# Kernel optimization log

Measured on AMD Instinct MI355X. Metric: run time of the kernel, lower is better.

The kernel has to match this reference:

```python
import jax, jax.numpy as jnp
import numpy as np

K = 16          # max_points
S = 3           # num_scales
DM = 256        # d_model
KD = 16         # k_dim geometric projection
TAU = 1e-4
LN_EPS = 1e-5


def _boundaries():
    edges = [(i, j) for i in range(K) for j in range(i + 1, K)]
    tris = [(i, j, k) for i in range(K) for j in range(i + 1, K) for k in range(j + 1, K)]
    E, T = len(edges), len(tris)
    B1 = np.zeros((K, E), np.float32)
    for e, (i, j) in enumerate(edges):
        B1[i, e] = -1.0
        B1[j, e] = 1.0
    eidx = {e: n for n, e in enumerate(edges)}
    B2 = np.zeros((E, T), np.float32)
    for t, (i, j, k) in enumerate(tris):
        B2[eidx[(j, k)], t] = 1.0
        B2[eidx[(i, k)], t] = -1.0
        B2[eidx[(i, j)], t] = 1.0
    ei = np.array([e[0] for e in edges])
    ej = np.array([e[1] for e in edges])
    tij = np.array([eidx[(a, b)] for a, b, c in tris])
    tjk = np.array([eidx[(b, c)] for a, b, c in tris])
    tik = np.array([eidx[(a, c)] for a, b, c in tris])
    return (jnp.asarray(B1), jnp.asarray(B2), jnp.asarray(np.abs(B1)),
            jnp.asarray(ei), jnp.asarray(ej), jnp.asarray(tij), jnp.asarray(tjk), jnp.asarray(tik))

_B1, _B2, _ABS, _EI, _EJ, _TIJ, _TJK, _TIK = _boundaries()
E = _B1.shape[1]  # 120


def _ln(x, g, b):
    m = jnp.mean(x, -1, keepdims=True)
    v = jnp.mean((x - m) ** 2, -1, keepdims=True)
    return (x - m) * jax.lax.rsqrt(v + LN_EPS) * g + b


def setup_inputs() -> dict:
    key = jax.random.key(0)
    ks = jax.random.split(key, 12)
    B = 1024
    p = lambda k, *sh: 0.02 * jax.random.normal(k, sh, dtype=jnp.float32)
    return {
        'x': jax.random.normal(ks[0], (B, K, DM), dtype=jnp.float32),
        'mask': jnp.ones((B, K), dtype=jnp.float32),
        'Wg': p(ks[1], DM, KD), 'bg': jnp.zeros((KD,), jnp.float32),
        'log_scales': jnp.linspace(-1.5, 1.5, S, dtype=jnp.float32),
        'Wv': p(ks[2], DM, DM * S), 'bv': jnp.zeros((DM * S,), jnp.float32),
        'We': p(ks[3], DM, DM * S), 'be': jnp.zeros((DM * S,), jnp.float32),
        'Wo': p(ks[4], DM * S * 2, DM), 'bo': jnp.zeros((DM,), jnp.float32),
        'ln1_g': jnp.ones((DM,), jnp.float32), 'ln1_b': jnp.zeros((DM,), jnp.float32),
        'ln2_g': jnp.ones((DM,), jnp.float32), 'ln2_b': jnp.zeros((DM,), jnp.float32),
        'Wf1': p(ks[5], DM, DM * 4), 'bf1': jnp.zeros((DM * 4,), jnp.float32),
        'Wf2': p(ks[6], DM * 4, DM), 'bf2': jnp.zeros((DM,), jnp.float32),
    }


def reference(x, mask, Wg, bg, log_scales, Wv, bv, We, be, Wo, bo,
              ln1_g, ln1_b, ln2_g, ln2_b, Wf1, bf1, Wf2, bf2):
    B = x.shape[0]
    xn = _ln(x, ln1_g, ln1_b)
    P = xn @ Wg + bg                                   # [B,K,KD]
    m2 = mask[:, :, None] * mask[:, None, :]           # [B,K,K]
    p2 = jnp.sum(P * P, -1)
    Dsq = jnp.maximum(p2[:, :, None] + p2[:, None, :] - 2.0 * jnp.einsum('bkc,blc->bkl', P, P), 0.0) * m2
    sig2 = jnp.exp(log_scales) ** 2                    # [S]
    V0 = (xn @ Wv + bv).reshape(B, K, S, DM).transpose(0, 2, 1, 3)   # [B,S,K,D]
    Eraw = jnp.einsum('ke,bkd->bed', _ABS, xn)         # [B,E,D]
    Ein = (Eraw @ We + be).reshape(B, E, S, DM).transpose(0, 2, 1, 3)  # [B,S,E,D]
    aff = jnp.exp(-Dsq[:, None] / (2.0 * sig2[None, :, None, None] + 1e-8)) * m2[:, None]  # [B,S,K,K]
    W1 = aff[:, :, _EI, _EJ]                           # [B,S,E]
    W2 = W1[:, :, _TIJ] * W1[:, :, _TJK] * W1[:, :, _TIK]  # [B,S,T]
    L0 = jnp.einsum('ke,bse,le->bskl', _B1, W1, _B1) + TAU * jnp.eye(K, dtype=x.dtype)
    node_upd = jnp.einsum('bskl,bsld->bskd', L0, V0)
    term_down = jnp.einsum('ke,bk,kf->bef', _B1, mask, _B1)
    term_up = jnp.einsum('et,bst,ft->bsef', _B2, W2, _B2)
    L1 = term_down[:, None] + term_up + TAU * jnp.eye(E, dtype=x.dtype)
    edge_msg = jnp.einsum('bsef,bsfd->bsed', L1, Ein)
    edge_upd = jnp.einsum('ke,bsed->bskd', _ABS, edge_msg)
    nu = node_upd.transpose(0, 2, 1, 3).reshape(B, K, S * DM)
    eu = edge_upd.transpose(0, 2, 1, 3).reshape(B, K, S * DM)
    x = x + (jnp.concatenate([nu, eu], -1) @ Wo + bo)  # residual + attn_out (dropout=eval noop)
    h = _ln(x, ln2_g, ln2_b)
    return x + (jax.nn.gelu(h @ Wf1 + bf1, approximate=False) @ Wf2 + bf2)
```

## Files before the change

kernel.cpp:

```cpp
#include <hip/hip_runtime.h>
#include <hip/hip_bf16.h>
#include <cstdint>
#include <cstddef>

#define TAU 1e-4f
#define LN_EPS 1e-5f

typedef unsigned short ushort_t;
typedef unsigned int uint_t;
typedef __attribute__((ext_vector_type(8))) short short8;
typedef __attribute__((ext_vector_type(4))) float f32x4;

__device__ __forceinline__ ushort_t f2bf(float f) {
    union { float f; unsigned int u; } c; c.f = f;
    unsigned int r = (c.u + 0x7fffu + ((c.u >> 16) & 1u)) >> 16;
    return (ushort_t)r;
}
__device__ __forceinline__ float bf2f(ushort_t u) {
    union { unsigned int u; float f; } c; c.u = ((unsigned int)u) << 16;
    return c.f;
}
__device__ __forceinline__ void glds16(const void* g, void* l) {
    __builtin_amdgcn_global_load_lds((const __attribute__((address_space(1))) unsigned int*)g,
                                     (__attribute__((address_space(3))) unsigned int*)l,
                                     16, 0, 0);
}

__global__ __launch_bounds__(256) void kprep(
    const float* __restrict__ Wv, const float* __restrict__ We,
    const float* __restrict__ Wo, const float* __restrict__ bv,
    const float* __restrict__ be, const float* __restrict__ Wf1,
    const float* __restrict__ Wf2, ushort_t* __restrict__ WkT,
    ushort_t* __restrict__ Wf1T, ushort_t* __restrict__ Wf2T,
    float* __restrict__ cvpart, float* __restrict__ beWo) {
    __shared__ __align__(16) float S[64 * 65];
    const int tid = threadIdx.x;
    const int id = blockIdx.x;
    if (id < 384) {
        float (*rowS)[256] = (float(*)[256])S;
        const int q0 = (id & 63) * 4;
        const int w = id >> 6;
        const int half = w / 3, s = w - half * 3;
        const float* src = half ? We : Wv;
#pragma unroll
        for (int r = 0; r < 4; ++r)
            rowS[r][tid] = src[(size_t)(q0 + r) * 768 + s * 256 + tid];
        __syncthreads();
        const float* wo = Wo + (size_t)(half * 768 + s * 256) * 256 + tid;
        float a0 = 0.f, a1 = 0.f, a2 = 0.f, a3 = 0.f;
        for (int d = 0; d < 256; ++d) {
            float wv = wo[(size_t)d * 256];
            a0 += rowS[0][d] * wv; a1 += rowS[1][d] * wv;
            a2 += rowS[2][d] * wv; a3 += rowS[3][d] * wv;
        }
        const int rt = half * 3 + s;
        ushort4 pk;
        pk.x = f2bf(a0); pk.y = f2bf(a1); pk.z = f2bf(a2); pk.w = f2bf(a3);
        *(ushort4*)&WkT[(size_t)(rt * 256 + tid) * 256 + q0] = pk;
    } else if (id < 390) {
        const int w = id - 384;
        const int half = w / 3, s = w - half * 3;
        const float* vec = half ? be : bv;
        S[tid] = vec[s * 256 + tid];
        __syncthreads();
        const float* wo = Wo + (size_t)(half * 768 + s * 256) * 256 + tid;
        float acc = 0.f;
        for (int d = 0; d < 256; ++d) acc += S[d] * wo[(size_t)d * 256];
        if (half) beWo[s * 256 + tid] = acc;
        else cvpart[s * 256 + tid] = acc;
    } else {
        float (*tS)[65] = (float(*)[65])S;
        const float* src; ushort_t* dst;
        int sr0, sc0, ss, dr0, dc0, ds_;
        if (id < 454) {
            int t = id - 390; int ki = t & 3, ni = t >> 2;
            src = Wf1; ss = 1024; sr0 = ki * 64; sc0 = ni * 64;
            dst = Wf1T; ds_ = 256; dr0 = ni * 64; dc0 = ki * 64;
        } else {
            int t = id - 454; int ki = t >> 2, ni = t & 3;
            src = Wf2; ss = 256; sr0 = ki * 64; sc0 = ni * 64;
            dst = Wf2T; ds_ = 1024; dr0 = ni * 64; dc0 = ki * 64;
        }
        const int rl = tid >> 6, cl = tid & 63;
#pragma unroll
        for (int p = 0; p < 16; ++p) {
            int r = p * 4 + rl;
            tS[r][cl] = src[(size_t)(sr0 + r) * ss + sc0 + cl];
        }
        __syncthreads();
#pragma unroll
        for (int p = 0; p < 16; ++p) {
            int r = p * 4 + rl;
            dst[(size_t)(dr0 + r) * ds_ + dc0 + cl] = f2bf(tS[cl][r]);
        }
    }
}

__global__ __launch_bounds__(256) void kLN1G(
    const float* __restrict__ xg, const float* __restrict__ maskg,
    const float* __restrict__ Wg, const float* __restrict__ bg,
    const float* __restrict__ ls, const float* __restrict__ g1,
    const float* __restrict__ b1, ushort_t* __restrict__ xnbuf,
    float* __restrict__ Mbuf, float* __restrict__ gbuf) {
    __shared__ float XS[16][260];
    __shared__ __align__(16) float WB[16 * 260];
    __shared__ float Pl[16][17];
    __shared__ float dotm[16][17];
    __shared__ float mk[16];
    float (*WgT)[260] = (float(*)[260])WB;
    float (*DsqS)[17] = (float(*)[17])WB;
    float (*Wh)[16][17] = (float(*)[16][17])(WB + 272);
    float* Ts = WB + 1088;
    const int b = blockIdx.x;
    const int tid = threadIdx.x;

    const float* xb = xg + (size_t)b * 4096;
#pragma unroll
    for (int i = 0; i < 4; ++i) {
        int idx = tid * 4 + i * 1024;
        int k = idx >> 8, c = idx & 255;
        float4 v = *(const float4*)&xb[idx];
        XS[k][c] = v.x; XS[k][c + 1] = v.y; XS[k][c + 2] = v.z; XS[k][c + 3] = v.w;
    }
    {
        const float4* wgp = (const float4*)(Wg + tid * 16);
        float4 w0 = wgp[0], w1 = wgp[1], w2 = wgp[2], w3 = wgp[3];
        WgT[0][tid] = w0.x; WgT[1][tid] = w0.y; WgT[2][tid] = w0.z; WgT[3][tid] = w0.w;
        WgT[4][tid] = w1.x; WgT[5][tid] = w1.y; WgT[6][tid] = w1.z; WgT[7][tid] = w1.w;
        WgT[8][tid] = w2.x; WgT[9][tid] = w2.y; WgT[10][tid] = w2.z; WgT[11][tid] = w2.w;
        WgT[12][tid] = w3.x; WgT[13][tid] = w3.y; WgT[14][tid] = w3.z; WgT[15][tid] = w3.w;
    }
    if (tid < 16) mk[tid] = maskg[b * 16 + tid];
    __syncthreads();

    {
        const int k = tid >> 4, c = tid & 15;
        float s = 0.f;
#pragma unroll
        for (int j = 0; j < 16; ++j) s += XS[k][c + 16 * j];
        for (int off = 8; off; off >>= 1) s += __shfl_down(s, off, 16);
        float mean = __shfl(s, 0, 16) * (1.f / 256.f);
        float vs = 0.f;
#pragma unroll
        for (int j = 0; j < 16; ++j) { float d = XS[k][c + 16 * j] - mean; vs += d * d; }
        for (int off = 8; off; off >>= 1) vs += __shfl_down(vs, off, 16);
        float rstd = rsqrtf(__shfl(vs, 0, 16) * (1.f / 256.f) + LN_EPS);
#pragma unroll
        for (int j = 0; j < 16; ++j) {
            int cc = c + 16 * j;
            XS[k][cc] = (XS[k][cc] - mean) * rstd * g1[cc] + b1[cc];
        }
    }
    __syncthreads();

#pragma unroll
    for (int i = 0; i < 8; ++i) {
        int idx2 = tid * 2 + i * 512;
        int k = idx2 >> 8, c = idx2 & 255;
        uint_t v = (uint_t)f2bf(XS[k][c]) | ((uint_t)f2bf(XS[k][c + 1]) << 16);
        *(uint_t*)&xnbuf[(size_t)b * 4096 + idx2] = v;
    }

    {
        const int k = tid >> 4, c = tid & 15;
        float acc = bg[c];
#pragma unroll
        for (int q4 = 0; q4 < 64; ++q4) {
            float4 wv = *(const float4*)&WgT[c][q4 * 4];
            float4 xv = *(const float4*)&XS[k][q4 * 4];
            acc += wv.x * xv.x + wv.y * xv.y + wv.z * xv.z + wv.w * xv.w;
        }
        Pl[k][c] = acc;
    }
    __syncthreads();
    const int k = tid >> 4, m = tid & 15;
    {
        float d = 0.f;
#pragma unroll
        for (int c = 0; c < 16; ++c) d += Pl[k][c] * Pl[m][c];
        dotm[k][m] = d;
    }
    __syncthreads();
    {
        float v = dotm[k][k] + dotm[m][m] - 2.f * dotm[k][m];
        DsqS[k][m] = fmaxf(v, 0.f) * mk[k] * mk[m];
    }
    {
        float d = DsqS[k][m];
        float mm = mk[k] * mk[m];
#pragma unroll
        for (int s = 0; s < 3; ++s) {
            float i2 = 1.f / (2.f * expf(2.f * ls[s]) + 1e-8f);
            Wh[s][k][m] = (k == m) ? 0.f : expf(-d * i2) * mm;
        }
    }
    __syncthreads();
    if (tid < 48) {
        int s = tid >> 4, j = tid & 15;
        float t = 0.f;
        for (int i = 0; i < j; ++i) {
            float d = 0.f;
            for (int jj = j + 1; jj < 16; ++jj) d += Wh[s][j][jj] * Wh[s][i][jj];
            t += Wh[s][i][j] * d;
        }
        Ts[s * 16 + j] = t;
    }
    __syncthreads();
    float gd = 0.f;
#pragma unroll
    for (int o = 0; o < 16; ++o) {
        if (o == m) continue;
        int u = o < m ? o : m, v = o < m ? m : o;
        float gu = (u == k) ? (float)(2 * k - 15) : ((u > k) ? 1.f : -1.f);
        float gv = (v == k) ? (float)(2 * k - 15) : ((v > k) ? 1.f : -1.f);
        gd += -gu * mk[u] + gv * mk[v];
        if (u == k || v == k) gd += TAU;
    }
    float* mb = Mbuf + (size_t)b * 1536;
#pragma unroll
    for (int s = 0; s < 3; ++s) {
        float rs = 0.f;
#pragma unroll
        for (int o = 0; o < 16; ++o) rs += Wh[s][k][o];
        float l0 = (k == m) ? (rs + TAU) : -Wh[s][k][m];
        float G = gd + ((k == m) ? 4.f * Ts[s * 16 + k] : 0.f);
        mb[s * 256 + tid] = l0;
        mb[768 + s * 256 + tid] = G;
        float gg = G;
        for (int off = 8; off; off >>= 1) gg += __shfl_down(gg, off, 16);
        if (m == 0) gbuf[b * 48 + k * 3 + s] = 0.5f * gg;
    }
}

__device__ __forceinline__ void gemm128(const ushort_t* __restrict__ A,
                                        const ushort_t* __restrict__ Bt,
                                        int Kdim, int m0, int n0,
                                        f32x4 acc[4][4],
                                        ushort_t (*As)[32], ushort_t (*Bs)[32]) {
    const int tid = threadIdx.x;
    const int wave = tid >> 6, lane = tid & 63;
    const int lq = lane >> 4, lr = lane & 15;
    const int wm = wave >> 1, wn = wave & 1;
    const int r = tid >> 2, ca = (tid & 3) << 3;
    const ushort_t* Ag0 = A + (size_t)(m0 + r) * Kdim + ca;
    const ushort_t* Ag1 = A + (size_t)(m0 + 64 + r) * Kdim + ca;
    const ushort_t* Bg0 = Bt + (size_t)(n0 + r) * Kdim + ca;
    const ushort_t* Bg1 = Bt + (size_t)(n0 + 64 + r) * Kdim + ca;
    char* AsD0 = (char*)As + wave * 1024;
    char* AsD1 = (char*)As + 4096 + wave * 1024;
    char* BsD0 = (char*)Bs + wave * 1024;
    char* BsD1 = (char*)Bs + 4096 + wave * 1024;
    for (int kt = 0; kt < Kdim; kt += 32) {
        __syncthreads();
        glds16(Ag0 + kt, AsD0);
        glds16(Ag1 + kt, AsD1);
        glds16(Bg0 + kt, BsD0);
        glds16(Bg1 + kt, BsD1);
        __syncthreads();
        short8 af[4], bfr[4];
#pragma unroll
        for (int i = 0; i < 4; ++i) af[i] = *(const short8*)&As[wm * 64 + i * 16 + lr][lq * 8];
#pragma unroll
        for (int j = 0; j < 4; ++j) bfr[j] = *(const short8*)&Bs[wn * 64 + j * 16 + lr][lq * 8];
#pragma unroll
        for (int i = 0; i < 4; ++i)
#pragma unroll
            for (int j = 0; j < 4; ++j)
                acc[i][j] = __builtin_amdgcn_mfma_f32_16x16x32_bf16(af[i], bfr[j], acc[i][j], 0, 0, 0);
    }
}

__device__ __forceinline__ void gemm64(const ushort_t* __restrict__ A,
                                       const ushort_t* __restrict__ Bt,
                                       int Kdim, int m0, int n0,
                                       f32x4 acc[2][4],
                                       ushort_t (*As)[32], ushort_t (*Bs)[32]) {
    const int tid = threadIdx.x;
    const int wave = tid >> 6, lane = tid & 63;
    const int lq = lane >> 4, lr = lane & 15;
    const int wm = wave >> 1, wn = wave & 1;
    const int r = tid >> 2, ca = (tid & 3) << 3;
    const ushort_t* Ag = A + (size_t)(m0 + r) * Kdim + ca;
    const ushort_t* Bg0 = Bt + (size_t)(n0 + r) * Kdim + ca;
    const ushort_t* Bg1 = Bt + (size_t)(n0 + 64 + r) * Kdim + ca;
    char* AsD = (char*)As + wave * 1024;
    char* Bs0D = (char*)Bs + wave * 1024;
    char* Bs1D = (char*)Bs + 4096 + wave * 1024;
    for (int kt = 0; kt < Kdim; kt += 32) {
        __syncthreads();
        glds16(Ag + kt, AsD);
        glds16(Bg0 + kt, Bs0D);
        glds16(Bg1 + kt, Bs1D);
        __syncthreads();
        short8 af[2], bfr[4];
#pragma unroll
        for (int i = 0; i < 2; ++i) af[i] = *(const short8*)&As[wm * 32 + i * 16 + lr][lq * 8];
#pragma unroll
        for (int j = 0; j < 4; ++j) bfr[j] = *(const short8*)&Bs[wn * 64 + j * 16 + lr][lq * 8];
#pragma unroll
        for (int i = 0; i < 2; ++i)
#pragma unroll
            for (int j = 0; j < 4; ++j)
                acc[i][j] = __builtin_amdgcn_mfma_f32_16x16x32_bf16(af[i], bfr[j], acc[i][j], 0, 0, 0);
    }
}

__global__ __launch_bounds__(256) void kY_gemm(const ushort_t* __restrict__ xn,
                                               const ushort_t* __restrict__ WkT,
                                               ushort_t* __restrict__ Y) {
    __shared__ ushort_t As[128][32];
    __shared__ ushort_t Bs[128][32];
    const int tid = threadIdx.x;
    const int m0 = blockIdx.x * 128, n0 = blockIdx.y * 128;
    f32x4 acc[4][4] = {};
    gemm128(xn, WkT, 256, m0, n0, acc, As, Bs);
    const int wave = tid >> 6, lane = tid & 63, lq = lane >> 4, lr = lane & 15;
    const int wm = wave >> 1, wn = wave & 1;
#pragma unroll
    for (int i = 0; i < 4; ++i)
#pragma unroll
        for (int j = 0; j < 4; ++j) {
            int n = n0 + wn * 64 + j * 16 + lr;
#pragma unroll
            for (int v = 0; v < 4; ++v) {
                int rg = m0 + wm * 64 + i * 16 + lq * 4 + v;
                Y[(size_t)rg * 1536 + n] = f2bf(acc[i][j][v]);
            }
        }
}

__global__ __launch_bounds__(256) void kZ_apply(
    const ushort_t* __restrict__ Y, const float* __restrict__ Mbuf,
    const float* __restrict__ xin, const float* __restrict__ bo,
    const float* __restrict__ cvpart, const float* __restrict__ beWo,
    const float* __restrict__ gbuf, const float* __restrict__ g2,
    const float* __restrict__ b2, float* __restrict__ xp,
    ushort_t* __restrict__ h) {
    __shared__ __align__(16) char YsRaw[49152];
    ushort_t* Ys = (ushort_t*)YsRaw;
    float (*xpS)[260] = (float(*)[260])YsRaw;
    __shared__ float Ms[1536];
    __shared__ float gS[48];
    __shared__ float mrS[16][2];
    const int b = blockIdx.x, tid = threadIdx.x;
    const int wave = tid >> 6, lane = tid & 63;
    const char* Ybc = (const char*)(Y + (size_t)b * 24576);
#pragma unroll
    for (int it = 0; it < 12; ++it) {
        int base = it * 4096 + wave * 1024;
        glds16(Ybc + base + lane * 16, YsRaw + base);
    }
#pragma unroll
    for (int i = 0; i < 6; ++i) Ms[tid + i * 256] = Mbuf[(size_t)b * 1536 + tid + i * 256];
    if (tid < 48) gS[tid] = gbuf[b * 48 + tid];
    __syncthreads();

    const int q = tid;
    float yv[96];
#pragma unroll
    for (int rt = 0; rt < 6; ++rt)
#pragma unroll
        for (int l = 0; l < 16; ++l)
            yv[rt * 16 + l] = bf2f(Ys[l * 1536 + rt * 256 + q]);

    float accv[16];
#pragma unroll
    for (int k = 0; k < 16; ++k) {
        float a = 0.f;
#pragma unroll
        for (int rt = 0; rt < 6; ++rt) {
            const float4* mp = (const float4*)&Ms[rt * 256 + k * 16];
            float4 m0 = mp[0], m1 = mp[1], m2 = mp[2], m3 = mp[3];
            const float* yp = &yv[rt * 16];
            a += m0.x * yp[0] + m0.y * yp[1] + m0.z * yp[2] + m0.w * yp[3]
               + m1.x * yp[4] + m1.y * yp[5] + m1.z * yp[6] + m1.w * yp[7]
               + m2.x * yp[8] + m2.y * yp[9] + m2.z * yp[10] + m2.w * yp[11]
               + m3.x * yp[12] + m3.y * yp[13] + m3.z * yp[14] + m3.w * yp[15];
        }
        accv[k] = a;
    }

    float cv = bo[q] + TAU * (cvpart[q] + cvpart[256 + q] + cvpart[512 + q]);
    float bw0 = beWo[q], bw1 = beWo[256 + q], bw2 = beWo[512 + q];
    const float* xb2 = xin + (size_t)b * 4096;
    float* xpb = xp + (size_t)b * 4096;
    float xpv[16];
#pragma unroll
    for (int k = 0; k < 16; ++k) {
        xpv[k] = accv[k] + xb2[k * 256 + q] + cv +
                 gS[k * 3] * bw0 + gS[k * 3 + 1] * bw1 + gS[k * 3 + 2] * bw2;
        xpb[k * 256 + q] = xpv[k];
    }
    __syncthreads();
#pragma unroll
    for (int k = 0; k < 16; ++k) xpS[k][q] = xpv[k];
    __syncthreads();

    {
        const int kk = tid >> 4, c = tid & 15;
        float s = 0.f;
#pragma unroll
        for (int j = 0; j < 16; ++j) s += xpS[kk][c + 16 * j];
        for (int off = 8; off; off >>= 1) s += __shfl_down(s, off, 16);
        float mean = __shfl(s, 0, 16) * (1.f / 256.f);
        float vs = 0.f;
#pragma unroll
        for (int j = 0; j < 16; ++j) { float d = xpS[kk][c + 16 * j] - mean; vs += d * d; }
        for (int off = 8; off; off >>= 1) vs += __shfl_down(vs, off, 16);
        float rstd = rsqrtf(__shfl(vs, 0, 16) * (1.f / 256.f) + LN_EPS);
        if (c == 0) { mrS[kk][0] = mean; mrS[kk][1] = rstd; }
    }
    __syncthreads();
    ushort_t* hb = h + (size_t)b * 4096;
    const float g2q = g2[q], b2q = b2[q];
#pragma unroll
    for (int k = 0; k < 16; ++k) {
        float m = mrS[k][0], r = mrS[k][1];
        hb[k * 256 + q] = f2bf((xpS[k][q] - m) * r * g2q + b2q);
    }
}

__global__ __launch_bounds__(256) void k3_gemm(const ushort_t* __restrict__ h,
                                               const ushort_t* __restrict__ Wf1T,
                                               const float* __restrict__ bf1,
                                               ushort_t* __restrict__ F1g) {
    __shared__ ushort_t As[128][32];
    __shared__ ushort_t Bs[128][32];
    const int tid = threadIdx.x;
    const int m0 = blockIdx.x * 128, n0 = blockIdx.y * 128;
    f32x4 acc[4][4] = {};
    gemm128(h, Wf1T, 256, m0, n0, acc, As, Bs);
    const int wave = tid >> 6, lane = tid & 63, lq = lane >> 4, lr = lane & 15;
    const int wm = wave >> 1, wn = wave & 1;
#pragma unroll
    for (int i = 0; i < 4; ++i)
#pragma unroll
        for (int j = 0; j < 4; ++j) {
            int n = n0 + wn * 64 + j * 16 + lr;
            float bn = bf1[n];
#pragma unroll
            for (int v = 0; v < 4; ++v) {
                int rg = m0 + wm * 64 + i * 16 + lq * 4 + v;
                float u = acc[i][j][v] + bn;
                float gl = 0.5f * u * (1.f + erff(u * 0.70710678118f));
                F1g[(size_t)rg * 1024 + n] = f2bf(gl);
            }
        }
}

__global__ __launch_bounds__(256) void k4_gemm(const ushort_t* __restrict__ F1g,
                                               const ushort_t* __restrict__ Wf2T,
                                               const float* __restrict__ bf2,
                                               const float* __restrict__ xp,
                                               float* __restrict__ out) {
    __shared__ ushort_t As[64][32];
    __shared__ ushort_t Bs[128][32];
    const int tid = threadIdx.x;
    const int m0 = blockIdx.x * 64, n0 = blockIdx.y * 128;
    f32x4 acc[2][4] = {};
    gemm64(F1g, Wf2T, 1024, m0, n0, acc, As, Bs);
    const int wave = tid >> 6, lane = tid & 63, lq = lane >> 4, lr = lane & 15;
    const int wm = wave >> 1, wn = wave & 1;
#pragma unroll
    for (int i = 0; i < 2; ++i)
#pragma unroll
        for (int j = 0; j < 4; ++j) {
            int n = n0 + wn * 64 + j * 16 + lr;
            float bn = bf2[n];
#pragma unroll
            for (int v = 0; v < 4; ++v) {
                size_t idx = (size_t)(m0 + wm * 32 + i * 16 + lq * 4 + v) * 256 + n;
                out[idx] = xp[idx] + acc[i][j][v] + bn;
            }
        }
}

extern "C" void kernel_launch(void* const* d_in, const int* in_sizes, int n_in,
                              void* d_out, int out_size, void* d_ws, size_t ws_size,
                              hipStream_t stream) {
    const float* x = (const float*)d_in[0];
    const float* mask = (const float*)d_in[1];
    const float* Wg = (const float*)d_in[2];
    const float* bg = (const float*)d_in[3];
    const float* ls = (const float*)d_in[4];
    const float* Wv = (const float*)d_in[5];
    const float* bv = (const float*)d_in[6];
    const float* We = (const float*)d_in[7];
    const float* be = (const float*)d_in[8];
    const float* Wo = (const float*)d_in[9];
    const float* bo = (const float*)d_in[10];
    const float* g1 = (const float*)d_in[11];
    const float* b1 = (const float*)d_in[12];
    const float* g2 = (const float*)d_in[13];
    const float* b2 = (const float*)d_in[14];
    const float* Wf1 = (const float*)d_in[15];
    const float* bf1 = (const float*)d_in[16];
    const float* Wf2 = (const float*)d_in[17];
    const float* bf2 = (const float*)d_in[18];
    float* out = (float*)d_out;

    char* ws = (char*)d_ws;
    ushort_t* Y = (ushort_t*)(ws);
    ushort_t* F1g = (ushort_t*)(ws);
    ushort_t* WkT = (ushort_t*)(ws + 50331648);
    ushort_t* Wf1T = (ushort_t*)(ws + 51118080);
    ushort_t* Wf2T = (ushort_t*)(ws + 51642368);
    float* cvpart = (float*)(ws + 52166656);
    float* beWo = (float*)(ws + 52169728);
    float* gbuf = (float*)(ws + 52172800);
    float* xp = (float*)(ws + 52369408);
    ushort_t* h = (ushort_t*)(ws + 69146624);
    ushort_t* xnbuf = (ushort_t*)(ws + 77535232);
    float* Mbuf = (float*)(ws + 85923840);

    kprep<<<dim3(518), dim3(256), 0, stream>>>(Wv, We, Wo, bv, be, Wf1, Wf2,
                                               WkT, Wf1T, Wf2T, cvpart, beWo);
    kLN1G<<<dim3(1024), dim3(256), 0, stream>>>(x, mask, Wg, bg, ls, g1, b1,
                                                xnbuf, Mbuf, gbuf);
    kY_gemm<<<dim3(128, 12), dim3(256), 0, stream>>>(xnbuf, WkT, Y);
    kZ_apply<<<dim3(1024), dim3(256), 0, stream>>>(Y, Mbuf, x, bo, cvpart, beWo, gbuf, g2, b2, xp, h);
    k3_gemm<<<dim3(128, 8), dim3(256), 0, stream>>>(h, Wf1T, bf1, F1g);
    k4_gemm<<<dim3(256, 2), dim3(256), 0, stream>>>(F1g, Wf2T, bf2, xp, out);
}
```

Before: 235.6 us.

## Reassociate attention: apply small K×K operators before the weight GEMM, merge prep kernels

Instead of computing Y = xn·Wk (K=256, N=1536) and then applying the per-batch 16×16 operators, each batch block first forms M·xn in registers and writes a [B*16, 1536] bf16 matrix. A single GEMM with K=1536 against the concatenated folded weights then produces the residual-added output directly. Weight preparation is merged into the LN1 kernel as extra blocks, and LN2 moves to a separate small kernel. This drops the xn buffer, the Y round trip, the Mbuf traffic and one launch, at the cost of a 6x longer GEMM reduction and a larger Mcat write.

```diff
diff --git a/kernel.cpp b/kernel.cpp
--- a/kernel.cpp
+++ b/kernel.cpp
@@ -16,103 +16,101 @@
     unsigned int r = (c.u + 0x7fffu + ((c.u >> 16) & 1u)) >> 16;
     return (ushort_t)r;
 }
-__device__ __forceinline__ float bf2f(ushort_t u) {
-    union { unsigned int u; float f; } c; c.u = ((unsigned int)u) << 16;
-    return c.f;
-}
 __device__ __forceinline__ void glds16(const void* g, void* l) {
     __builtin_amdgcn_global_load_lds((const __attribute__((address_space(1))) unsigned int*)g,
                                      (__attribute__((address_space(3))) unsigned int*)l,
                                      16, 0, 0);
 }
 
-__global__ __launch_bounds__(256) void kprep(
+__global__ __launch_bounds__(256) void kA(
+    const float* __restrict__ xg, const float* __restrict__ maskg,
+    const float* __restrict__ Wg, const float* __restrict__ bg,
+    const float* __restrict__ ls, const float* __restrict__ g1,
+    const float* __restrict__ b1, ushort_t* __restrict__ Mcat,
+    float* __restrict__ gbuf,
     const float* __restrict__ Wv, const float* __restrict__ We,
     const float* __restrict__ Wo, const float* __restrict__ bv,
     const float* __restrict__ be, const float* __restrict__ Wf1,
-    const float* __restrict__ Wf2, ushort_t* __restrict__ WkT,
+    const float* __restrict__ Wf2, ushort_t* __restrict__ WcatT,
     ushort_t* __restrict__ Wf1T, ushort_t* __restrict__ Wf2T,
     float* __restrict__ cvpart, float* __restrict__ beWo) {
-    __shared__ __align__(16) float S[64 * 65];
-    const int tid = threadIdx.x;
-    const int id = blockIdx.x;
-    if (id < 384) {
-        float (*rowS)[256] = (float(*)[256])S;
-        const int q0 = (id & 63) * 4;
-        const int w = id >> 6;
-        const int half = w / 3, s = w - half * 3;
-        const float* src = half ? We : Wv;
-#pragma unroll
-        for (int r = 0; r < 4; ++r)
-            rowS[r][tid] = src[(size_t)(q0 + r) * 768 + s * 256 + tid];
-        __syncthreads();
-        const float* wo = Wo + (size_t)(half * 768 + s * 256) * 256 + tid;
-        float a0 = 0.f, a1 = 0.f, a2 = 0.f, a3 = 0.f;
-        for (int d = 0; d < 256; ++d) {
-            float wv = wo[(size_t)d * 256];
-            a0 += rowS[0][d] * wv; a1 += rowS[1][d] * wv;
-            a2 += rowS[2][d] * wv; a3 += rowS[3][d] * wv;
-        }
-        const int rt = half * 3 + s;
-        ushort4 pk;
-        pk.x = f2bf(a0); pk.y = f2bf(a1); pk.z = f2bf(a2); pk.w = f2bf(a3);
-        *(ushort4*)&WkT[(size_t)(rt * 256 + tid) * 256 + q0] = pk;
-    } else if (id < 390) {
-        const int w = id - 384;
-        const int half = w / 3, s = w - half * 3;
-        const float* vec = half ? be : bv;
-        S[tid] = vec[s * 256 + tid];
-        __syncthreads();
-        const float* wo = Wo + (size_t)(half * 768 + s * 256) * 256 + tid;
-        float acc = 0.f;
-        for (int d = 0; d < 256; ++d) acc += S[d] * wo[(size_t)d * 256];
-        if (half) beWo[s * 256 + tid] = acc;
-        else cvpart[s * 256 + tid] = acc;
-    } else {
-        float (*tS)[65] = (float(*)[65])S;
-        const float* src; ushort_t* dst;
-        int sr0, sc0, ss, dr0, dc0, ds_;
-        if (id < 454) {
-            int t = id - 390; int ki = t & 3, ni = t >> 2;
-            src = Wf1; ss = 1024; sr0 = ki * 64; sc0 = ni * 64;
-            dst = Wf1T; ds_ = 256; dr0 = ni * 64; dc0 = ki * 64;
+    __shared__ __align__(16) float POOL[9872];
+    const int tid = threadIdx.x;
+
+    if (blockIdx.x >= 1024) {
+        const int id = blockIdx.x - 1024;
+        if (id < 384) {
+            float (*rowS)[256] = (float(*)[256])POOL;
+            const int q0 = (id & 63) * 4;
+            const int w = id >> 6;
+            const int half = w / 3, s = w - half * 3;
+            const float* src = half ? We : Wv;
+#pragma unroll
+            for (int r = 0; r < 4; ++r)
+                rowS[r][tid] = src[(size_t)(q0 + r) * 768 + s * 256 + tid];
+            __syncthreads();
+            const float* wo = Wo + (size_t)(half * 768 + s * 256) * 256 + tid;
+            float a0 = 0.f, a1 = 0.f, a2 = 0.f, a3 = 0.f;
+            for (int d = 0; d < 256; ++d) {
+                float wv = wo[(size_t)d * 256];
+                a0 += rowS[0][d] * wv; a1 += rowS[1][d] * wv;
+                a2 += rowS[2][d] * wv; a3 += rowS[3][d] * wv;
+            }
+            const int rt = half * 3 + s;
+            ushort4 pk;
+            pk.x = f2bf(a0); pk.y = f2bf(a1); pk.z = f2bf(a2); pk.w = f2bf(a3);
+            *(ushort4*)&WcatT[(size_t)tid * 1536 + rt * 256 + q0] = pk;
+        } else if (id < 390) {
+            const int w = id - 384;
+            const int half = w / 3, s = w - half * 3;
+            const float* vec = half ? be : bv;
+            POOL[tid] = vec[s * 256 + tid];
+            __syncthreads();
+            const float* wo = Wo + (size_t)(half * 768 + s * 256) * 256 + tid;
+            float acc = 0.f;
+            for (int d = 0; d < 256; ++d) acc += POOL[d] * wo[(size_t)d * 256];
+            if (half) beWo[s * 256 + tid] = acc;
+            else cvpart[s * 256 + tid] = acc;
         } else {
-            int t = id - 454; int ki = t >> 2, ni = t & 3;
-            src = Wf2; ss = 256; sr0 = ki * 64; sc0 = ni * 64;
-            dst = Wf2T; ds_ = 1024; dr0 = ni * 64; dc0 = ki * 64;
-        }
-        const int rl = tid >> 6, cl = tid & 63;
-#pragma unroll
-        for (int p = 0; p < 16; ++p) {
-            int r = p * 4 + rl;
-            tS[r][cl] = src[(size_t)(sr0 + r) * ss + sc0 + cl];
-        }
-        __syncthreads();
-#pragma unroll
-        for (int p = 0; p < 16; ++p) {
-            int r = p * 4 + rl;
-            dst[(size_t)(dr0 + r) * ds_ + dc0 + cl] = f2bf(tS[cl][r]);
-        }
-    }
-}
-
-__global__ __launch_bounds__(256) void kLN1G(
-    const float* __restrict__ xg, const float* __restrict__ maskg,
-    const float* __restrict__ Wg, const float* __restrict__ bg,
-    const float* __restrict__ ls, const float* __restrict__ g1,
-    const float* __restrict__ b1, ushort_t* __restrict__ xnbuf,
-    float* __restrict__ Mbuf, float* __restrict__ gbuf) {
-    __shared__ float XS[16][260];
-    __shared__ __align__(16) float WB[16 * 260];
-    __shared__ float Pl[16][17];
-    __shared__ float dotm[16][17];
-    __shared__ float mk[16];
+            float (*tS)[65] = (float(*)[65])POOL;
+            const float* src; ushort_t* dst;
+            int sr0, sc0, ss, dr0, dc0, ds_;
+            if (id < 454) {
+                int t = id - 390; int ki = t & 3, ni = t >> 2;
+                src = Wf1; ss = 1024; sr0 = ki * 64; sc0 = ni * 64;
+                dst = Wf1T; ds_ = 256; dr0 = ni * 64; dc0 = ki * 64;
+            } else {
+                int t = id - 454; int ki = t >> 2, ni = t & 3;
+                src = Wf2; ss = 256; sr0 = ki * 64; sc0 = ni * 64;
+                dst = Wf2T; ds_ = 1024; dr0 = ni * 64; dc0 = ki * 64;
+            }
+            const int rl = tid >> 6, cl = tid & 63;
+#pragma unroll
+            for (int p = 0; p < 16; ++p) {
+                int r = p * 4 + rl;
+                tS[r][cl] = src[(size_t)(sr0 + r) * ss + sc0 + cl];
+            }
+            __syncthreads();
+#pragma unroll
+            for (int p = 0; p < 16; ++p) {
+                int r = p * 4 + rl;
+                dst[(size_t)(dr0 + r) * ds_ + dc0 + cl] = f2bf(tS[cl][r]);
+            }
+        }
+        return;
+    }
+
+    const int b = blockIdx.x;
+    float (*XS)[260] = (float(*)[260])POOL;
+    float* WB = POOL + 4160;
+    float (*Pl)[17] = (float(*)[17])(POOL + 8320);
+    float (*dotm)[17] = (float(*)[17])(POOL + 8592);
+    float* Ms = POOL + 8320;
+    float* mk = POOL + 9856;
     float (*WgT)[260] = (float(*)[260])WB;
     float (*DsqS)[17] = (float(*)[17])WB;
     float (*Wh)[16][17] = (float(*)[16][17])(WB + 272);
     float* Ts = WB + 1088;
-    const int b = blockIdx.x;
-    const int tid = threadIdx.x;
 
     const float* xb = xg + (size_t)b * 4096;
 #pragma unroll
@@ -152,14 +150,6 @@
         }
     }
     __syncthreads();
-
-#pragma unroll
-    for (int i = 0; i < 8; ++i) {
-        int idx2 = tid * 2 + i * 512;
-        int k = idx2 >> 8, c = idx2 & 255;
-        uint_t v = (uint_t)f2bf(XS[k][c]) | ((uint_t)f2bf(XS[k][c + 1]) << 16);
-        *(uint_t*)&xnbuf[(size_t)b * 4096 + idx2] = v;
-    }
 
     {
         const int k = tid >> 4, c = tid & 15;
@@ -216,7 +206,6 @@
         gd += -gu * mk[u] + gv * mk[v];
         if (u == k || v == k) gd += TAU;
     }
-    float* mb = Mbuf + (size_t)b * 1536;
 #pragma unroll
     for (int s = 0; s < 3; ++s) {
         float rs = 0.f;
@@ -224,11 +213,40 @@
         for (int o = 0; o < 16; ++o) rs += Wh[s][k][o];
         float l0 = (k == m) ? (rs + TAU) : -Wh[s][k][m];
         float G = gd + ((k == m) ? 4.f * Ts[s * 16 + k] : 0.f);
-        mb[s * 256 + tid] = l0;
-        mb[768 + s * 256 + tid] = G;
+        Ms[s * 256 + tid] = l0;
+        Ms[768 + s * 256 + tid] = G;
         float gg = G;
         for (int off = 8; off; off >>= 1) gg += __shfl_down(gg, off, 16);
         if (m == 0) gbuf[b * 48 + k * 3 + s] = 0.5f * gg;
+    }
+    __syncthreads();
+
+    {
+        const int q2 = (tid & 127) * 2;
+        const int rtbase = (tid >> 7) * 3;
+        float xv0[16], xv1[16];
+#pragma unroll
+        for (int l = 0; l < 16; ++l) { xv0[l] = XS[l][q2]; xv1[l] = XS[l][q2 + 1]; }
+        const size_t obase = (size_t)b * 16 * 1536;
+#pragma unroll
+        for (int rtt = 0; rtt < 3; ++rtt) {
+            const int rt = rtbase + rtt;
+#pragma unroll
+            for (int kk = 0; kk < 16; ++kk) {
+                const float4* mp = (const float4*)&Ms[rt * 256 + kk * 16];
+                float4 m0 = mp[0], m1 = mp[1], m2 = mp[2], m3 = mp[3];
+                float a0 = m0.x * xv0[0] + m0.y * xv0[1] + m0.z * xv0[2] + m0.w * xv0[3]
+                         + m1.x * xv0[4] + m1.y * xv0[5] + m1.z * xv0[6] + m1.w * xv0[7]
+                         + m2.x * xv0[8] + m2.y * xv0[9] + m2.z * xv0[10] + m2.w * xv0[11]
+                         + m3.x * xv0[12] + m3.y * xv0[13] + m3.z * xv0[14] + m3.w * xv0[15];
+                float a1 = m0.x * xv1[0] + m0.y * xv1[1] + m0.z * xv1[2] + m0.w * xv1[3]
+                         + m1.x * xv1[4] + m1.y * xv1[5] + m1.z * xv1[6] + m1.w * xv1[7]
+                         + m2.x * xv1[8] + m2.y * xv1[9] + m2.z * xv1[10] + m2.w * xv1[11]
+                         + m3.x * xv1[12] + m3.y * xv1[13] + m3.z * xv1[14] + m3.w * xv1[15];
+                uint_t pk = (uint_t)f2bf(a0) | ((uint_t)f2bf(a1) << 16);
+                *(uint_t*)&Mcat[obase + (size_t)kk * 1536 + rt * 256 + q2] = pk;
+            }
+        }
     }
 }
 
@@ -305,119 +323,65 @@
     }
 }
 
-__global__ __launch_bounds__(256) void kY_gemm(const ushort_t* __restrict__ xn,
-                                               const ushort_t* __restrict__ WkT,
-                                               ushort_t* __restrict__ Y) {
-    __shared__ ushort_t As[128][32];
+__global__ __launch_bounds__(256) void kZY_gemm(
+    const ushort_t* __restrict__ Mcat, const ushort_t* __restrict__ WcatT,
+    const float* __restrict__ xin, const float* __restrict__ bo,
+    const float* __restrict__ cvpart, const float* __restrict__ beWo,
+    const float* __restrict__ gbuf, float* __restrict__ xp) {
+    __shared__ ushort_t As[64][32];
     __shared__ ushort_t Bs[128][32];
-    const int tid = threadIdx.x;
-    const int m0 = blockIdx.x * 128, n0 = blockIdx.y * 128;
-    f32x4 acc[4][4] = {};
-    gemm128(xn, WkT, 256, m0, n0, acc, As, Bs);
+    __shared__ float cvS[128], bewS[3][128], gblk[64][3];
+    const int tid = threadIdx.x;
+    const int m0 = blockIdx.x * 64, n0 = blockIdx.y * 128;
+    if (tid < 128) {
+        int n = n0 + tid;
+        cvS[tid] = bo[n] + TAU * (cvpart[n] + cvpart[256 + n] + cvpart[512 + n]);
+        bewS[0][tid] = beWo[n];
+        bewS[1][tid] = beWo[256 + n];
+        bewS[2][tid] = beWo[512 + n];
+    }
+    if (tid < 192) { int rr = tid / 3, s = tid - rr * 3; gblk[rr][s] = gbuf[(size_t)(m0 + rr) * 3 + s]; }
+    f32x4 acc[2][4] = {};
+    gemm64(Mcat, WcatT, 1536, m0, n0, acc, As, Bs);
     const int wave = tid >> 6, lane = tid & 63, lq = lane >> 4, lr = lane & 15;
     const int wm = wave >> 1, wn = wave & 1;
 #pragma unroll
-    for (int i = 0; i < 4; ++i)
+    for (int i = 0; i < 2; ++i)
 #pragma unroll
         for (int j = 0; j < 4; ++j) {
-            int n = n0 + wn * 64 + j * 16 + lr;
+            int nl = wn * 64 + j * 16 + lr;
 #pragma unroll
             for (int v = 0; v < 4; ++v) {
-                int rg = m0 + wm * 64 + i * 16 + lq * 4 + v;
-                Y[(size_t)rg * 1536 + n] = f2bf(acc[i][j][v]);
-            }
-        }
-}
-
-__global__ __launch_bounds__(256) void kZ_apply(
-    const ushort_t* __restrict__ Y, const float* __restrict__ Mbuf,
-    const float* __restrict__ xin, const float* __restrict__ bo,
-    const float* __restrict__ cvpart, const float* __restrict__ beWo,
-    const float* __restrict__ gbuf, const float* __restrict__ g2,
-    const float* __restrict__ b2, float* __restrict__ xp,
-    ushort_t* __restrict__ h) {
-    __shared__ __align__(16) char YsRaw[49152];
-    ushort_t* Ys = (ushort_t*)YsRaw;
-    float (*xpS)[260] = (float(*)[260])YsRaw;
-    __shared__ float Ms[1536];
-    __shared__ float gS[48];
-    __shared__ float mrS[16][2];
-    const int b = blockIdx.x, tid = threadIdx.x;
-    const int wave = tid >> 6, lane = tid & 63;
-    const char* Ybc = (const char*)(Y + (size_t)b * 24576);
-#pragma unroll
-    for (int it = 0; it < 12; ++it) {
-        int base = it * 4096 + wave * 1024;
-        glds16(Ybc + base + lane * 16, YsRaw + base);
-    }
-#pragma unroll
-    for (int i = 0; i < 6; ++i) Ms[tid + i * 256] = Mbuf[(size_t)b * 1536 + tid + i * 256];
-    if (tid < 48) gS[tid] = gbuf[b * 48 + tid];
-    __syncthreads();
-
-    const int q = tid;
-    float yv[96];
-#pragma unroll
-    for (int rt = 0; rt < 6; ++rt)
-#pragma unroll
-        for (int l = 0; l < 16; ++l)
-            yv[rt * 16 + l] = bf2f(Ys[l * 1536 + rt * 256 + q]);
-
-    float accv[16];
-#pragma unroll
-    for (int k = 0; k < 16; ++k) {
-        float a = 0.f;
-#pragma unroll
-        for (int rt = 0; rt < 6; ++rt) {
-            const float4* mp = (const float4*)&Ms[rt * 256 + k * 16];
-            float4 m0 = mp[0], m1 = mp[1], m2 = mp[2], m3 = mp[3];
-            const float* yp = &yv[rt * 16];
-            a += m0.x * yp[0] + m0.y * yp[1] + m0.z * yp[2] + m0.w * yp[3]
-               + m1.x * yp[4] + m1.y * yp[5] + m1.z * yp[6] + m1.w * yp[7]
-               + m2.x * yp[8] + m2.y * yp[9] + m2.z * yp[10] + m2.w * yp[11]
-               + m3.x * yp[12] + m3.y * yp[13] + m3.z * yp[14] + m3.w * yp[15];
-        }
-        accv[k] = a;
-    }
-
-    float cv = bo[q] + TAU * (cvpart[q] + cvpart[256 + q] + cvpart[512 + q]);
-    float bw0 = beWo[q], bw1 = beWo[256 + q], bw2 = beWo[512 + q];
-    const float* xb2 = xin + (size_t)b * 4096;
-    float* xpb = xp + (size_t)b * 4096;
-    float xpv[16];
-#pragma unroll
-    for (int k = 0; k < 16; ++k) {
-        xpv[k] = accv[k] + xb2[k * 256 + q] + cv +
-                 gS[k * 3] * bw0 + gS[k * 3 + 1] * bw1 + gS[k * 3 + 2] * bw2;
-        xpb[k * 256 + q] = xpv[k];
-    }
-    __syncthreads();
-#pragma unroll
-    for (int k = 0; k < 16; ++k) xpS[k][q] = xpv[k];
-    __syncthreads();
-
-    {
-        const int kk = tid >> 4, c = tid & 15;
-        float s = 0.f;
-#pragma unroll
-        for (int j = 0; j < 16; ++j) s += xpS[kk][c + 16 * j];
-        for (int off = 8; off; off >>= 1) s += __shfl_down(s, off, 16);
-        float mean = __shfl(s, 0, 16) * (1.f / 256.f);
-        float vs = 0.f;
-#pragma unroll
-        for (int j = 0; j < 16; ++j) { float d = xpS[kk][c + 16 * j] - mean; vs += d * d; }
-        for (int off = 8; off; off >>= 1) vs += __shfl_down(vs, off, 16);
-        float rstd = rsqrtf(__shfl(vs, 0, 16) * (1.f / 256.f) + LN_EPS);
-        if (c == 0) { mrS[kk][0] = mean; mrS[kk][1] = rstd; }
-    }
-    __syncthreads();
-    ushort_t* hb = h + (size_t)b * 4096;
-    const float g2q = g2[q], b2q = b2[q];
-#pragma unroll
-    for (int k = 0; k < 16; ++k) {
-        float m = mrS[k][0], r = mrS[k][1];
-        hb[k * 256 + q] = f2bf((xpS[k][q] - m) * r * g2q + b2q);
-    }
+                int rl = wm * 32 + i * 16 + lq * 4 + v;
+                size_t idx = (size_t)(m0 + rl) * 256 + n0 + nl;
+                xp[idx] = acc[i][j][v] + xin[idx] + cvS[nl] +
+                          gblk[rl][0] * bewS[0][nl] + gblk[rl][1] * bewS[1][nl] +
+                          gblk[rl][2] * bewS[2][nl];
+            }
+        }
+}
+
+__global__ __launch_bounds__(256) void k_ln2(const float* __restrict__ xp,
+                                             const float* __restrict__ g2,
+                                             const float* __restrict__ b2,
+                                             ushort_t* __restrict__ h) {
+    const int tid = threadIdx.x;
+    const int row = blockIdx.x * 4 + (tid >> 6);
+    const int lane = tid & 63;
+    const float* xr = xp + (size_t)row * 256;
+    float v0 = xr[lane], v1 = xr[lane + 64], v2 = xr[lane + 128], v3 = xr[lane + 192];
+    float s = v0 + v1 + v2 + v3;
+    for (int m = 32; m; m >>= 1) s += __shfl_xor(s, m, 64);
+    float mean = s * (1.f / 256.f);
+    float d0 = v0 - mean, d1 = v1 - mean, d2 = v2 - mean, d3 = v3 - mean;
+    float q = d0 * d0 + d1 * d1 + d2 * d2 + d3 * d3;
+    for (int m = 32; m; m >>= 1) q += __shfl_xor(q, m, 64);
+    float rstd = rsqrtf(q * (1.f / 256.f) + LN_EPS);
+    ushort_t* hr = h + (size_t)row * 256;
+    hr[lane] = f2bf(d0 * rstd * g2[lane] + b2[lane]);
+    hr[lane + 64] = f2bf(d1 * rstd * g2[lane + 64] + b2[lane + 64]);
+    hr[lane + 128] = f2bf(d2 * rstd * g2[lane + 128] + b2[lane + 128]);
+    hr[lane + 192] = f2bf(d3 * rstd * g2[lane + 192] + b2[lane + 192]);
 }
 
 __global__ __launch_bounds__(256) void k3_gemm(const ushort_t* __restrict__ h,
@@ -500,9 +464,9 @@
     float* out = (float*)d_out;
 
     char* ws = (char*)d_ws;
-    ushort_t* Y = (ushort_t*)(ws);
+    ushort_t* Mcat = (ushort_t*)(ws);
     ushort_t* F1g = (ushort_t*)(ws);
-    ushort_t* WkT = (ushort_t*)(ws + 50331648);
+    ushort_t* WcatT = (ushort_t*)(ws + 50331648);
     ushort_t* Wf1T = (ushort_t*)(ws + 51118080);
     ushort_t* Wf2T = (ushort_t*)(ws + 51642368);
     float* cvpart = (float*)(ws + 52166656);
@@ -510,15 +474,13 @@
     float* gbuf = (float*)(ws + 52172800);
     float* xp = (float*)(ws + 52369408);
     ushort_t* h = (ushort_t*)(ws + 69146624);
-    ushort_t* xnbuf = (ushort_t*)(ws + 77535232);
-    float* Mbuf = (float*)(ws + 85923840);
-
-    kprep<<<dim3(518), dim3(256), 0, stream>>>(Wv, We, Wo, bv, be, Wf1, Wf2,
-                                               WkT, Wf1T, Wf2T, cvpart, beWo);
-    kLN1G<<<dim3(1024), dim3(256), 0, stream>>>(x, mask, Wg, bg, ls, g1, b1,
-                                                xnbuf, Mbuf, gbuf);
-    kY_gemm<<<dim3(128, 12), dim3(256), 0, stream>>>(xnbuf, WkT, Y);
-    kZ_apply<<<dim3(1024), dim3(256), 0, stream>>>(Y, Mbuf, x, bo, cvpart, beWo, gbuf, g2, b2, xp, h);
+
+    kA<<<dim3(1542), dim3(256), 0, stream>>>(x, mask, Wg, bg, ls, g1, b1,
+                                             Mcat, gbuf,
+                                             Wv, We, Wo, bv, be, Wf1, Wf2,
+                                             WcatT, Wf1T, Wf2T, cvpart, beWo);
+    kZY_gemm<<<dim3(256, 2), dim3(256), 0, stream>>>(Mcat, WcatT, x, bo, cvpart, beWo, gbuf, xp);
+    k_ln2<<<dim3(4096), dim3(256), 0, stream>>>(xp, g2, b2, h);
     k3_gemm<<<dim3(128, 8), dim3(256), 0, stream>>>(h, Wf1T, bf1, F1g);
     k4_gemm<<<dim3(256, 2), dim3(256), 0, stream>>>(F1g, Wf2T, bf2, xp, out);
 }
```

Result: faster. 221.3 us (-6.1%).
